# Kernel tuning notes

Measured on AMD Instinct MI355X. Metric: run time of the kernel, lower is better.

The kernel has to match this reference:

```python
import jax, jax.numpy as jnp
import numpy as np

QP_ITERS = 500          # projected-gradient iterations on the dual (converges for this tiny QP)
S_PEN = 1000.0          # slack penalty from the cvxpy objective
BN_EPS = 1e-5


def batchnorm(x, gamma, beta):
    # x: (B, N, C); BatchNorm1d training-mode stats over (batch, points)
    mu = x.mean(axis=(0, 1))
    var = x.var(axis=(0, 1))
    return (x - mu) * jax.lax.rsqrt(var + BN_EPS) * gamma + beta


def solve_qp(p, G, h):
    # min_z,s 0.5||z-p||^2 + 1000||s||^2  s.t. G z <= h + s, s >= 0
    # Dual (eliminating z = p - G^T lam, s = lam/(2*1000)):
    #   min_{lam>=0} 0.5 lam^T M lam - lam^T q,  M = G G^T + I/(2*S_PEN), q = G p - h
    nc = G.shape[1]
    M = jnp.einsum('bcv,bdv->bcd', G, G) + jnp.eye(nc, dtype=G.dtype) / (2.0 * S_PEN)
    q = jnp.einsum('bcv,bv->bc', G, p) - h
    # safe step size: 1/trace(M) <= 1/lambda_max(M)
    alpha = jax.lax.stop_gradient(1.0 / jnp.trace(M, axis1=1, axis2=2))[:, None]

    def step(lam, _):
        grad = jnp.einsum('bcd,bd->bc', M, lam) - q
        return jnp.maximum(lam - alpha * grad, 0.0), None

    lam0 = jnp.zeros_like(q)
    lam, _ = jax.lax.scan(step, lam0, None, length=QP_ITERS)
    z = p - jnp.einsum('bcv,bc->bv', G, lam)
    return z


def setup_inputs() -> dict:
    key = jax.random.key(0)
    ks = jax.random.split(key, 16)
    B, N, NC = 64, 8192, 12

    def w(k, shape, s):
        return (jax.random.normal(k, shape) * s).astype(jnp.float32)

    bc2 = jnp.concatenate([w(ks[10], (NC * 3,), 0.02), jnp.full((NC,), 0.02, jnp.float32)])
    return {
        'pcd': jax.random.normal(ks[0], (B, N, 3), dtype=jnp.float32),
        # MiniPointNet (1x1 convs as matmuls) + batchnorm affine params
        'W1': w(ks[1], (64, 3), 0.4), 'b1': jnp.zeros(64), 'g1': jnp.ones(64), 'be1': jnp.zeros(64),
        'W2': w(ks[2], (128, 64), 0.1), 'b2': jnp.zeros(128), 'g2': jnp.ones(128), 'be2': jnp.zeros(128),
        'W3': w(ks[3], (256, 128), 0.07), 'b3': jnp.zeros(256), 'g3': jnp.ones(256), 'be3': jnp.zeros(256),
        'Wfc': w(ks[4], (128, 256), 0.05), 'bfc': jnp.zeros(128),
        # constraint_net: 128 -> 128 -> 48
        'Wc1': w(ks[5], (128, 128), 0.08), 'bc1': jnp.zeros(128),
        'Wc2': w(ks[6], (NC * 4, 128), 0.08), 'bc2': bc2,
        # p_net: 128 -> 64 -> 7 (last layer ~N(0, 0.001), zero bias)
        'Wp1': w(ks[7], (64, 128), 0.08), 'bp1': jnp.zeros(64),
        'Wp2': w(ks[8], (7, 64), 0.001), 'bp2': jnp.zeros(7),
    }


def reference(pcd, W1, b1, g1, be1, W2, b2, g2, be2, W3, b3, g3, be3,
              Wfc, bfc, Wc1, bc1, Wc2, bc2, Wp1, bp1, Wp2, bp2):
    B = pcd.shape[0]
    NC = bc2.shape[0] // 4
    # MiniPointNet: pointwise MLP + global max pool
    x = jax.nn.relu(batchnorm(pcd @ W1.T + b1, g1, be1))     # (B,N,64)
    x = jax.nn.relu(batchnorm(x @ W2.T + b2, g2, be2))       # (B,N,128)
    x = jax.nn.relu(batchnorm(x @ W3.T + b3, g3, be3))       # (B,N,256)
    feats = x.max(axis=1) @ Wfc.T + bfc                       # (B,128)

    raw_p = jax.nn.relu(feats @ Wp1.T + bp1) @ Wp2.T + bp2    # (B,7)
    p_pred = jnp.concatenate([
        jnp.tanh(raw_p[:, :3]) * 0.1,
        jnp.tanh(raw_p[:, 3:6]) * 1.57,
        jnp.tanh(raw_p[:, 6:7]) * 0.05], axis=1)

    out_cons = (jax.nn.relu(feats @ Wc1.T + bc1) @ Wc2.T + bc2).reshape(B, NC, 4)
    normals = out_cons[:, :, :3]
    # F.normalize(p=2, dim=2): clamp norm at 1e-12
    normals = normals / jnp.clip(jnp.linalg.norm(normals, axis=2, keepdims=True), 1e-12)
    h = jax.nn.softplus(out_cons[:, :, 3]) + 0.005            # (B,NC)
    G = jnp.concatenate([normals, jnp.zeros((B, NC, 4), normals.dtype)], axis=2)  # (B,NC,7)

    delta_norm = solve_qp(p_pred, G, h)                       # (B,7)
    return delta_norm, normals, h, p_pred
```

## Files before the change

kernel.cpp:

```cpp
#include <hip/hip_runtime.h>
#include <hip/hip_bf16.h>

#define NPTS 524288
#define NBATCH 64

typedef __attribute__((ext_vector_type(8))) short bf16x8;
typedef __attribute__((ext_vector_type(4))) float f32x4;
typedef const float* __restrict__ fp;

__device__ __forceinline__ __hip_bfloat16 f2b(float v) { return __float2bfloat16(v); }
__device__ __forceinline__ unsigned bfbits(float v) {
    union { __hip_bfloat16 h; unsigned short s; } u; u.h = f2b(v); return (unsigned)u.s;
}

__device__ __forceinline__ unsigned fkey(float f) {
    unsigned u = __float_as_uint(f);
    return u ^ ((u & 0x80000000u) ? 0xFFFFFFFFu : 0x80000000u);
}
__device__ __forceinline__ float funkey(unsigned k) {
    unsigned u = (k & 0x80000000u) ? (k ^ 0x80000000u) : ~k;
    return __uint_as_float(u);
}

union U8 { bf16x8 v; __hip_bfloat16 e[8]; unsigned u[4]; };

static __device__ __forceinline__ f32x4 mfma16(bf16x8 a, bf16x8 b, f32x4 c) {
    return __builtin_amdgcn_mfma_f32_16x16x32_bf16(a, b, c, 0, 0, 0);
}

__global__ void k_prep(fp W1, fp b1, fp W2, fp W3,
                       __hip_bfloat16* __restrict__ W2b,
                       __hip_bfloat16* __restrict__ W3b,
                       unsigned* __restrict__ W1p )
{
    int i = blockIdx.x * blockDim.x + threadIdx.x;
    if (i < 8192) W2b[i] = f2b(W2[i]);
    const int j = i - 8192;
    if (j >= 0 && j < 32768) W3b[j] = f2b(W3[j]);
    const int c = i - 40960;
    if (c >= 0 && c < 64) {
        unsigned lo = bfbits(W1[3*c+0]) | (bfbits(W1[3*c+1]) << 16);
        unsigned hi = bfbits(W1[3*c+2]) | (bfbits(b1[c]) << 16);
        W1p[c*2+0] = lo; W1p[c*2+1] = hi;
    }
}

__launch_bounds__(256)
__global__ void k_moments(fp pcd, float* __restrict__ mom)
{
    float s[9];
#pragma unroll
    for (int i = 0; i < 9; ++i) s[i] = 0.f;
    const int stride = gridDim.x * blockDim.x;
    for (int p = blockIdx.x * blockDim.x + threadIdx.x; p < NPTS; p += stride) {
        const float x = pcd[3*p+0], y = pcd[3*p+1], z = pcd[3*p+2];
        s[0] += x; s[1] += y; s[2] += z;
        s[3] = fmaf(x, x, s[3]); s[4] = fmaf(x, y, s[4]); s[5] = fmaf(x, z, s[5]);
        s[6] = fmaf(y, y, s[6]); s[7] = fmaf(y, z, s[7]); s[8] = fmaf(z, z, s[8]);
    }
#pragma unroll
    for (int off = 1; off < 64; off <<= 1) {
#pragma unroll
        for (int i = 0; i < 9; ++i) s[i] += __shfl_xor(s[i], off);
    }
    __shared__ float red[4][9];
    const int lane = threadIdx.x & 63, wv = threadIdx.x >> 6;
    if (lane == 0) {
#pragma unroll
        for (int i = 0; i < 9; ++i) red[wv][i] = s[i];
    }
    __syncthreads();
    if (threadIdx.x < 9) {
        const int i = threadIdx.x;
        atomicAdd(&mom[i], red[0][i] + red[1][i] + red[2][i] + red[3][i]);
    }
}

__global__ void k_fin1(const float* __restrict__ mom, fp W1, fp b1, fp g1, fp be1,
                       float* __restrict__ s1, float* __restrict__ t1)
{
    const int c = threadIdx.x;
    const float inv = 1.f / (float)NPTS;
    const float m0 = mom[0]*inv, m1 = mom[1]*inv, m2 = mom[2]*inv;
    const float c00 = mom[3]*inv - m0*m0, c01 = mom[4]*inv - m0*m1, c02 = mom[5]*inv - m0*m2;
    const float c11 = mom[6]*inv - m1*m1, c12 = mom[7]*inv - m1*m2, c22 = mom[8]*inv - m2*m2;
    const float w0 = W1[c*3+0], w1 = W1[c*3+1], w2 = W1[c*3+2];
    const float mu = w0*m0 + w1*m1 + w2*m2 + b1[c];
    float var = w0*w0*c00 + w1*w1*c11 + w2*w2*c22 + 2.f*(w0*w1*c01 + w0*w2*c02 + w1*w2*c12);
    var = fmaxf(var, 0.f);
    const float sc = g1[c] * rsqrtf(var + 1e-5f);
    s1[c] = sc;
    t1[c] = be1[c] - mu*sc;
}

__launch_bounds__(256, 2)
__global__ void k_pass1(fp pcd, const unsigned* __restrict__ W1p,
                        const float* __restrict__ s1, const float* __restrict__ t1,
                        const __hip_bfloat16* __restrict__ W2b,
                        float* __restrict__ st2s, float* __restrict__ st2q)
{
    __shared__ __hip_bfloat16 x1s[64*72];
    const int tid = threadIdx.x, wv = tid >> 6, lane = tid & 63;
    const int m = lane & 15, q = lane >> 4;
    const int batch = blockIdx.x >> 5, sub = blockIdx.x & 31;

    bf16x8 wb1[4];
#pragma unroll
    for (int nt = 0; nt < 4; ++nt) {
        U8 w; w.u[0] = w.u[1] = w.u[2] = w.u[3] = 0;
        if (q == 0) { w.u[0] = W1p[(nt*16+m)*2]; w.u[1] = W1p[(nt*16+m)*2+1]; }
        wb1[nt] = w.v;
    }
    float s1v[4], t1v[4];
#pragma unroll
    for (int nt = 0; nt < 4; ++nt) { s1v[nt] = s1[nt*16+m]; t1v[nt] = t1[nt*16+m]; }

    bf16x8 wb2[8][2];
#pragma unroll
    for (int nt = 0; nt < 8; ++nt) {
#pragma unroll
        for (int kk = 0; kk < 2; ++kk)
            wb2[nt][kk] = *(const bf16x8*)(W2b + (nt*16+m)*64 + kk*32 + q*8);
    }

    float s_acc[8], q_acc[8];
#pragma unroll
    for (int nt = 0; nt < 8; ++nt) { s_acc[nt] = 0.f; q_acc[nt] = 0.f; }

    const int rowA = (wv*16 + m) * 72;

    for (int it = 0; it < 4; ++it) {
        const int p0 = batch*8192 + sub*256 + it*64 + wv*16;
        const float* pp = pcd + (size_t)(p0 + m) * 3;
        const float cx = pp[0], cy = pp[1], cz = pp[2];
        U8 a1; a1.u[0] = a1.u[1] = a1.u[2] = a1.u[3] = 0;
        if (q == 0) {
            a1.u[0] = bfbits(cx) | (bfbits(cy) << 16);
            a1.u[1] = bfbits(cz) | (bfbits(1.f) << 16);
        }
#pragma unroll
        for (int nt = 0; nt < 4; ++nt) {
            f32x4 c1 = mfma16(a1.v, wb1[nt], (f32x4){0.f,0.f,0.f,0.f});
#pragma unroll
            for (int r = 0; r < 4; ++r) {
                const float v = fmaxf(fmaf(c1[r], s1v[nt], t1v[nt]), 0.f);
                const unsigned own = bfbits(v);
                const unsigned oth = (unsigned)__shfl_xor((int)own, 1);
                if ((m & 1) == 0) {
                    const int row = wv*16 + q*4 + r;
                    *(unsigned*)&x1s[row*72 + nt*16 + m] = own | (oth << 16);
                }
            }
        }
        const bf16x8 a2k0 = *(const bf16x8*)&x1s[rowA + 0  + q*8];
        const bf16x8 a2k1 = *(const bf16x8*)&x1s[rowA + 32 + q*8];
#pragma unroll
        for (int nt = 0; nt < 8; ++nt) {
            f32x4 c = mfma16(a2k0, wb2[nt][0], (f32x4){0.f,0.f,0.f,0.f});
            c = mfma16(a2k1, wb2[nt][1], c);
            s_acc[nt] += (c[0] + c[1]) + (c[2] + c[3]);
            q_acc[nt] = fmaf(c[0],c[0], fmaf(c[1],c[1], fmaf(c[2],c[2], fmaf(c[3],c[3], q_acc[nt]))));
        }
    }
#pragma unroll
    for (int nt = 0; nt < 8; ++nt) {
        s_acc[nt] += __shfl_xor(s_acc[nt], 16); q_acc[nt] += __shfl_xor(q_acc[nt], 16);
        s_acc[nt] += __shfl_xor(s_acc[nt], 32); q_acc[nt] += __shfl_xor(q_acc[nt], 32);
    }
    __syncthreads();
    float* red = (float*)x1s;
    if (q == 0) {
#pragma unroll
        for (int nt = 0; nt < 8; ++nt) {
            red[wv*128 + nt*16 + m] = s_acc[nt];
            red[512 + wv*128 + nt*16 + m] = q_acc[nt];
        }
    }
    __syncthreads();
    if (tid < 128) {
        float s = 0.f, ss = 0.f;
#pragma unroll
        for (int w4 = 0; w4 < 4; ++w4) { s += red[w4*128 + tid]; ss += red[512 + w4*128 + tid]; }
        const int slot = blockIdx.x & 255;
        atomicAdd(&st2s[slot*128 + tid], s);
        atomicAdd(&st2q[slot*128 + tid], ss);
    }
}

__global__ void k_fin2(const float* __restrict__ sum, const float* __restrict__ sq,
                       fp g, fp be, float* __restrict__ sOut, float* __restrict__ tOut)
{
    const int ch = threadIdx.x;
    float s = 0.f, ss = 0.f;
    for (int slot = 0; slot < 256; ++slot) { s += sum[slot*128 + ch]; ss += sq[slot*128 + ch]; }
    const float inv = 1.f / (float)NPTS;
    const float mu = s * inv;
    const float var = fmaxf(ss * inv - mu*mu, 0.f);
    const float sc = g[ch] * rsqrtf(var + 1e-5f);
    sOut[ch] = sc;
    tOut[ch] = be[ch] - mu*sc;
}

__launch_bounds__(256, 2)
__global__ void k_pass2(fp pcd, const unsigned* __restrict__ W1p,
                        const float* __restrict__ s1, const float* __restrict__ t1,
                        const __hip_bfloat16* __restrict__ W2b,
                        const float* __restrict__ s2, const float* __restrict__ t2,
                        const __hip_bfloat16* __restrict__ W3b,
                        float* __restrict__ st3s, float* __restrict__ st3q,
                        unsigned* __restrict__ maxk, unsigned* __restrict__ mink)
{
    __shared__ __hip_bfloat16 x1s[64*72];
    __shared__ __hip_bfloat16 x2s[64*136];
    __shared__ __hip_bfloat16 w2s[128*72];
    const int tid = threadIdx.x, wv = tid >> 6, lane = tid & 63;
    const int m = lane & 15, q = lane >> 4;
    const int batch = blockIdx.x >> 5, sub = blockIdx.x & 31;

    {
        const int row = tid >> 1, half = tid & 1;
#pragma unroll
        for (int jj = 0; jj < 2; ++jj) {
            const bf16x8 wa = *(const bf16x8*)(W2b + row*64 + half*32 + jj*16);
            const bf16x8 wb = *(const bf16x8*)(W2b + row*64 + half*32 + jj*16 + 8);
            *(bf16x8*)&w2s[row*72 + half*32 + jj*16]     = wa;
            *(bf16x8*)&w2s[row*72 + half*32 + jj*16 + 8] = wb;
        }
    }

    bf16x8 wb1[4];
#pragma unroll
    for (int nt = 0; nt < 4; ++nt) {
        U8 w; w.u[0] = w.u[1] = w.u[2] = w.u[3] = 0;
        if (q == 0) { w.u[0] = W1p[(nt*16+m)*2]; w.u[1] = W1p[(nt*16+m)*2+1]; }
        wb1[nt] = w.v;
    }
    float s1v[4], t1v[4];
#pragma unroll
    for (int nt = 0; nt < 4; ++nt) { s1v[nt] = s1[nt*16+m]; t1v[nt] = t1[nt*16+m]; }
    float s2v[8], t2v[8];
#pragma unroll
    for (int nt = 0; nt < 8; ++nt) { s2v[nt] = s2[nt*16+m]; t2v[nt] = t2[nt*16+m]; }

    bf16x8 wb3[4][4];
#pragma unroll
    for (int nt = 0; nt < 4; ++nt) {
        const int ch3 = wv*64 + nt*16 + m;
#pragma unroll
        for (int ks = 0; ks < 4; ++ks)
            wb3[nt][ks] = *(const bf16x8*)(W3b + ch3*128 + ks*32 + q*8);
    }

    float s3[4], q3[4], mx3[4], mn3[4];
#pragma unroll
    for (int nt = 0; nt < 4; ++nt) { s3[nt]=0.f; q3[nt]=0.f; mx3[nt]=-3.4e38f; mn3[nt]=3.4e38f; }

    const int rowA = (wv*16 + m) * 72;
    __syncthreads();

    for (int it = 0; it < 4; ++it) {
        asm volatile("" ::: "memory");
        const int p0 = batch*8192 + sub*256 + it*64 + wv*16;
        const float* pp = pcd + (size_t)(p0 + m) * 3;
        const float cx = pp[0], cy = pp[1], cz = pp[2];
        U8 a1; a1.u[0] = a1.u[1] = a1.u[2] = a1.u[3] = 0;
        if (q == 0) {
            a1.u[0] = bfbits(cx) | (bfbits(cy) << 16);
            a1.u[1] = bfbits(cz) | (bfbits(1.f) << 16);
        }
#pragma unroll
        for (int nt = 0; nt < 4; ++nt) {
            f32x4 c1 = mfma16(a1.v, wb1[nt], (f32x4){0.f,0.f,0.f,0.f});
#pragma unroll
            for (int r = 0; r < 4; ++r) {
                const float v = fmaxf(fmaf(c1[r], s1v[nt], t1v[nt]), 0.f);
                const unsigned own = bfbits(v);
                const unsigned oth = (unsigned)__shfl_xor((int)own, 1);
                if ((m & 1) == 0) {
                    const int row = wv*16 + q*4 + r;
                    *(unsigned*)&x1s[row*72 + nt*16 + m] = own | (oth << 16);
                }
            }
        }
        const bf16x8 a2k0 = *(const bf16x8*)&x1s[rowA + 0  + q*8];
        const bf16x8 a2k1 = *(const bf16x8*)&x1s[rowA + 32 + q*8];
#pragma unroll
        for (int nt = 0; nt < 8; ++nt) {
            const bf16x8 wb20 = *(const bf16x8*)&w2s[(nt*16+m)*72 + 0  + q*8];
            const bf16x8 wb21 = *(const bf16x8*)&w2s[(nt*16+m)*72 + 32 + q*8];
            f32x4 c = mfma16(a2k0, wb20, (f32x4){0.f,0.f,0.f,0.f});
            c = mfma16(a2k1, wb21, c);
#pragma unroll
            for (int r = 0; r < 4; ++r) {
                const float v = fmaxf(fmaf(c[r], s2v[nt], t2v[nt]), 0.f);
                const unsigned own = bfbits(v);
                const unsigned oth = (unsigned)__shfl_xor((int)own, 1);
                if ((m & 1) == 0) {
                    const int row = wv*16 + q*4 + r;
                    *(unsigned*)&x2s[row*136 + nt*16 + m] = own | (oth << 16);
                }
            }
        }
        __syncthreads();
#pragma unroll
        for (int ms = 0; ms < 4; ++ms) {
            const int rowM = (ms*16 + m) * 136;
            bf16x8 a3[4];
#pragma unroll
            for (int ks = 0; ks < 4; ++ks)
                a3[ks] = *(const bf16x8*)&x2s[rowM + ks*32 + q*8];
#pragma unroll
            for (int nt = 0; nt < 4; ++nt) {
                f32x4 c = mfma16(a3[0], wb3[nt][0], (f32x4){0.f,0.f,0.f,0.f});
                c = mfma16(a3[1], wb3[nt][1], c);
                c = mfma16(a3[2], wb3[nt][2], c);
                c = mfma16(a3[3], wb3[nt][3], c);
                s3[nt] += (c[0] + c[1]) + (c[2] + c[3]);
                q3[nt] = fmaf(c[0],c[0], fmaf(c[1],c[1], fmaf(c[2],c[2], fmaf(c[3],c[3], q3[nt]))));
                mx3[nt] = fmaxf(fmaxf(c[0], c[1]), fmaxf(fmaxf(c[2], c[3]), mx3[nt]));
                mn3[nt] = fminf(fminf(c[0], c[1]), fminf(fminf(c[2], c[3]), mn3[nt]));
            }
        }
        __syncthreads();
    }
#pragma unroll
    for (int nt = 0; nt < 4; ++nt) {
        s3[nt] += __shfl_xor(s3[nt], 16);  q3[nt] += __shfl_xor(q3[nt], 16);
        mx3[nt] = fmaxf(mx3[nt], __shfl_xor(mx3[nt], 16));
        mn3[nt] = fminf(mn3[nt], __shfl_xor(mn3[nt], 16));
        s3[nt] += __shfl_xor(s3[nt], 32);  q3[nt] += __shfl_xor(q3[nt], 32);
        mx3[nt] = fmaxf(mx3[nt], __shfl_xor(mx3[nt], 32));
        mn3[nt] = fminf(mn3[nt], __shfl_xor(mn3[nt], 32));
    }
    if (q == 0) {
        const int slot = blockIdx.x & 255;
#pragma unroll
        for (int nt = 0; nt < 4; ++nt) {
            const int ch3 = wv*64 + nt*16 + m;
            atomicAdd(&st3s[slot*256 + ch3], s3[nt]);
            atomicAdd(&st3q[slot*256 + ch3], q3[nt]);
            atomicMax(&maxk[batch*256 + ch3], fkey(mx3[nt]));
            atomicMin(&mink[batch*256 + ch3], fkey(mn3[nt]));
        }
    }
}

__global__ void k_fin3(const float* __restrict__ sum, const float* __restrict__ sq,
                       fp g, fp be, const unsigned* __restrict__ maxk,
                       const unsigned* __restrict__ mink, float* __restrict__ pre)
{
    const int ch = threadIdx.x;
    float s = 0.f, ss = 0.f;
    for (int slot = 0; slot < 256; ++slot) { s += sum[slot*256 + ch]; ss += sq[slot*256 + ch]; }
    const float inv = 1.f / (float)NPTS;
    const float mu = s * inv;
    const float var = fmaxf(ss * inv - mu*mu, 0.f);
    const float sc = g[ch] * rsqrtf(var + 1e-5f);
    const float sh = be[ch] - mu*sc;
    for (int b = 0; b < NBATCH; ++b) {
        const float fmx = funkey(maxk[b*256 + ch]);
        const float fmn = funkey(mink[b*256 + ch]);
        const float pick = (sc >= 0.f) ? fmx : fmn;
        pre[b*256 + ch] = fmaxf(fmaf(pick, sc, sh), 0.f);
    }
}

__launch_bounds__(128)
__global__ void k_head(const float* __restrict__ pre,
                       fp Wfc, fp bfc, fp Wc1, fp bc1, fp Wc2, fp bc2,
                       fp Wp1, fp bp1, fp Wp2, fp bp2,
                       float* __restrict__ out)
{
    __shared__ float pf[256], ft[128], hcs[128], hps[64], ocs[48], nrm[36], hS[12], pp[8];
    const int bb = blockIdx.x, tid = threadIdx.x;
    pf[tid] = pre[bb*256 + tid];
    pf[tid+128] = pre[bb*256 + 128 + tid];
    __syncthreads();
    {
        float a = bfc[tid];
        const float* wr = Wfc + tid*256;
        for (int k = 0; k < 256; ++k) a = fmaf(pf[k], wr[k], a);
        ft[tid] = a;
    }
    __syncthreads();
    {
        float a = bc1[tid];
        const float* wr = Wc1 + tid*128;
        for (int k = 0; k < 128; ++k) a = fmaf(ft[k], wr[k], a);
        hcs[tid] = fmaxf(a, 0.f);
    }
    if (tid < 64) {
        float a = bp1[tid];
        const float* wr = Wp1 + tid*128;
        for (int k = 0; k < 128; ++k) a = fmaf(ft[k], wr[k], a);
        hps[tid] = fmaxf(a, 0.f);
    }
    __syncthreads();
    if (tid < 48) {
        float a = bc2[tid];
        const float* wr = Wc2 + tid*128;
        for (int k = 0; k < 128; ++k) a = fmaf(hcs[k], wr[k], a);
        ocs[tid] = a;
    }
    if (tid < 7) {
        float a = bp2[tid];
        const float* wr = Wp2 + tid*64;
        for (int k = 0; k < 64; ++k) a = fmaf(hps[k], wr[k], a);
        const float sc = (tid < 3) ? 0.1f : ((tid < 6) ? 1.57f : 0.05f);
        pp[tid] = tanhf(a) * sc;
    }
    __syncthreads();
    if (tid < 12) {
        float nx = ocs[tid*4+0], ny = ocs[tid*4+1], nz = ocs[tid*4+2];
        const float nn = fmaxf(sqrtf(nx*nx + ny*ny + nz*nz), 1e-12f);
        const float inv = 1.f / nn;
        nx *= inv; ny *= inv; nz *= inv;
        nrm[tid*3+0] = nx; nrm[tid*3+1] = ny; nrm[tid*3+2] = nz;
        const float xx = ocs[tid*4+3];
        hS[tid] = ((xx > 20.f) ? xx : log1pf(expf(xx))) + 0.005f;
    }
    __syncthreads();

    const int lane = tid & 63;
    const int c = (lane < 12) ? lane : 11;
    const float n0 = nrm[c*3+0], n1 = nrm[c*3+1], n2 = nrm[c*3+2];
    float Mrow[12];
    float trace = 0.f;
#pragma unroll
    for (int d = 0; d < 12; ++d) {
        const float d0 = nrm[d*3+0], d1 = nrm[d*3+1], d2 = nrm[d*3+2];
        Mrow[d] = n0*d0 + n1*d1 + n2*d2 + ((d == lane) ? 5e-4f : 0.f);
        trace += d0*d0 + d1*d1 + d2*d2;
    }
    const float alpha = 1.f / (trace + 12.f*5e-4f);
    const float qc = n0*pp[0] + n1*pp[1] + n2*pp[2] - hS[c];
    float lam = 0.f;
    for (int it = 0; it < 500; ++it) {
        const float l0 = __shfl(lam, 0),  l1 = __shfl(lam, 1),  l2 = __shfl(lam, 2);
        const float l3 = __shfl(lam, 3),  l4 = __shfl(lam, 4),  l5 = __shfl(lam, 5);
        const float l6 = __shfl(lam, 6),  l7 = __shfl(lam, 7),  l8 = __shfl(lam, 8);
        const float l9 = __shfl(lam, 9),  l10 = __shfl(lam, 10), l11 = __shfl(lam, 11);
        const float g0 = fmaf(Mrow[0], l0, fmaf(Mrow[3], l3, fmaf(Mrow[6], l6, Mrow[9]*l9)));
        const float g1 = fmaf(Mrow[1], l1, fmaf(Mrow[4], l4, fmaf(Mrow[7], l7, Mrow[10]*l10)));
        const float g2 = fmaf(Mrow[2], l2, fmaf(Mrow[5], l5, fmaf(Mrow[8], l8, Mrow[11]*l11)));
        lam = fmaxf(fmaf(-alpha, g0 + g1 + g2 - qc, lam), 0.f);
    }
    float v0 = (lane < 12) ? n0*lam : 0.f;
    float v1 = (lane < 12) ? n1*lam : 0.f;
    float v2 = (lane < 12) ? n2*lam : 0.f;
#pragma unroll
    for (int off = 1; off <= 8; off <<= 1) {
        v0 += __shfl_xor(v0, off);
        v1 += __shfl_xor(v1, off);
        v2 += __shfl_xor(v2, off);
    }
    if (tid < 7) {
        float z;
        if (tid == 0) z = pp[0] - v0;
        else if (tid == 1) z = pp[1] - v1;
        else if (tid == 2) z = pp[2] - v2;
        else z = pp[tid];
        out[bb*7 + tid] = z;
    }
    if (tid < 36) out[448 + bb*36 + tid] = nrm[tid];
    if (tid < 12) out[2752 + bb*12 + tid] = hS[tid];
    if (tid < 7)  out[3520 + bb*7 + tid] = pp[tid];
}

extern "C" void kernel_launch(void* const* d_in, const int* in_sizes, int n_in,
                              void* d_out, int out_size, void* d_ws, size_t ws_size,
                              hipStream_t stream) {
    fp pcd = (fp)d_in[0];
    fp W1 = (fp)d_in[1],  b1 = (fp)d_in[2],  g1 = (fp)d_in[3],  be1 = (fp)d_in[4];
    fp W2 = (fp)d_in[5],  b2 = (fp)d_in[6],  g2 = (fp)d_in[7],  be2 = (fp)d_in[8];
    fp W3 = (fp)d_in[9],  b3 = (fp)d_in[10], g3 = (fp)d_in[11], be3 = (fp)d_in[12];
    fp Wfc = (fp)d_in[13], bfc = (fp)d_in[14];
    fp Wc1 = (fp)d_in[15], bc1 = (fp)d_in[16];
    fp Wc2 = (fp)d_in[17], bc2 = (fp)d_in[18];
    fp Wp1 = (fp)d_in[19], bp1 = (fp)d_in[20];
    fp Wp2 = (fp)d_in[21], bp2 = (fp)d_in[22];
    (void)b2; (void)b3;

    float* ws = (float*)d_ws;
    float* mom  = ws + 0;
    float* s1   = ws + 16;
    float* t1   = ws + 80;
    float* s2   = ws + 144;
    float* t2   = ws + 272;
    float* pre  = ws + 400;
    float* st2s = ws + 16784;
    float* st2q = ws + 49552;
    float* st3s = ws + 82320;
    float* st3q = ws + 147856;
    unsigned* maxk = (unsigned*)(ws + 213392);
    unsigned* mink = (unsigned*)(ws + 229776);
    __hip_bfloat16* W2b = (__hip_bfloat16*)(ws + 246160);
    __hip_bfloat16* W3b = (__hip_bfloat16*)(ws + 250256);
    unsigned* W1p = (unsigned*)(ws + 266640);
    if (ws_size < (size_t)266768 * 4) return;

    hipMemsetAsync(d_ws, 0, (size_t)229776 * 4, stream);
    hipMemsetAsync((void*)mink, 0xFF, (size_t)16384 * 4, stream);

    k_prep<<<161, 256, 0, stream>>>(W1, b1, W2, W3, W2b, W3b, W1p);
    k_moments<<<256, 256, 0, stream>>>(pcd, mom);
    k_fin1<<<1, 64, 0, stream>>>(mom, W1, b1, g1, be1, s1, t1);
    k_pass1<<<2048, 256, 0, stream>>>(pcd, W1p, s1, t1, W2b, st2s, st2q);
    k_fin2<<<1, 128, 0, stream>>>(st2s, st2q, g2, be2, s2, t2);
    k_pass2<<<2048, 256, 0, stream>>>(pcd, W1p, s1, t1, W2b, s2, t2, W3b,
                                      st3s, st3q, maxk, mink);
    k_fin3<<<1, 256, 0, stream>>>(st3s, st3q, g3, be3, maxk, mink, pre);
    k_head<<<64, 128, 0, stream>>>(pre, Wfc, bfc, Wc1, bc1, Wc2, bc2,
                                   Wp1, bp1, Wp2, bp2, (float*)d_out);
}
```

Measured before the change: 328.6 us.

## Fold BN1 into W1, redistribute layer-1 output via shuffles, fuse fin3 into head

Folds the layer-1 batchnorm scale and shift into the packed bf16 W1 weights inside k_fin1. Layer 1 is computed with swapped MFMA operands and its output is redistributed to layer-2 A-fragments through cross-lane shuffles instead of an LDS round trip. k_pass2 now keeps W2 in registers, double-buffers the x2 LDS tile and drops the per-iteration barrier. Other changes: fewer atomic slots for the BN statistics (smaller memset and reduction), k_fin3 merged into k_head, and more k_moments blocks. Register pressure rises (pass1 now asks for 3 blocks per SM), and folding the scale before the bf16 rounding slightly changes numerics.

```diff
diff --git a/kernel.cpp b/kernel.cpp
--- a/kernel.cpp
+++ b/kernel.cpp
@@ -12,6 +12,9 @@
 __device__ __forceinline__ unsigned bfbits(float v) {
     union { __hip_bfloat16 h; unsigned short s; } u; u.h = f2b(v); return (unsigned)u.s;
 }
+__device__ __forceinline__ unsigned pk2(float a, float b) {
+    return bfbits(a) | (bfbits(b) << 16);
+}
 
 __device__ __forceinline__ unsigned fkey(float f) {
     unsigned u = __float_as_uint(f);
@@ -28,21 +31,13 @@
     return __builtin_amdgcn_mfma_f32_16x16x32_bf16(a, b, c, 0, 0, 0);
 }
 
-__global__ void k_prep(fp W1, fp b1, fp W2, fp W3,
-                       __hip_bfloat16* __restrict__ W2b,
-                       __hip_bfloat16* __restrict__ W3b,
-                       unsigned* __restrict__ W1p )
+__global__ void k_prep(fp W2, fp W3, __hip_bfloat16* __restrict__ W2b,
+                       __hip_bfloat16* __restrict__ W3b)
 {
     int i = blockIdx.x * blockDim.x + threadIdx.x;
     if (i < 8192) W2b[i] = f2b(W2[i]);
     const int j = i - 8192;
     if (j >= 0 && j < 32768) W3b[j] = f2b(W3[j]);
-    const int c = i - 40960;
-    if (c >= 0 && c < 64) {
-        unsigned lo = bfbits(W1[3*c+0]) | (bfbits(W1[3*c+1]) << 16);
-        unsigned hi = bfbits(W1[3*c+2]) | (bfbits(b1[c]) << 16);
-        W1p[c*2+0] = lo; W1p[c*2+1] = hi;
-    }
 }
 
 __launch_bounds__(256)
@@ -77,7 +72,7 @@
 }
 
 __global__ void k_fin1(const float* __restrict__ mom, fp W1, fp b1, fp g1, fp be1,
-                       float* __restrict__ s1, float* __restrict__ t1)
+                       unsigned* __restrict__ W1p)
 {
     const int c = threadIdx.x;
     const float inv = 1.f / (float)NPTS;
@@ -89,17 +84,39 @@
     float var = w0*w0*c00 + w1*w1*c11 + w2*w2*c22 + 2.f*(w0*w1*c01 + w0*w2*c02 + w1*w2*c12);
     var = fmaxf(var, 0.f);
     const float sc = g1[c] * rsqrtf(var + 1e-5f);
-    s1[c] = sc;
-    t1[c] = be1[c] - mu*sc;
-}
-
-__launch_bounds__(256, 2)
+    const float sh = be1[c] - mu*sc;
+    W1p[c*2+0] = pk2(w0*sc, w1*sc);
+    W1p[c*2+1] = pk2(w2*sc, b1[c]*sc + sh);
+}
+
+#define L1_AND_REDIST(a2f)                                                      \
+    {                                                                           \
+        unsigned u1s[4][2];                                                     \
+        _Pragma("unroll")                                                       \
+        for (int nt = 0; nt < 4; ++nt) {                                        \
+            f32x4 c1 = mfma16(wb1[nt], a1.v, (f32x4){0.f,0.f,0.f,0.f});         \
+            u1s[nt][0] = pk2(fmaxf(c1[0],0.f), fmaxf(c1[1],0.f));               \
+            u1s[nt][1] = pk2(fmaxf(c1[2],0.f), fmaxf(c1[3],0.f));               \
+        }                                                                       \
+        const int srcBase = m + ((q & 1) ? 32 : 0);                             \
+        _Pragma("unroll")                                                       \
+        for (int ks = 0; ks < 2; ++ks) {                                        \
+            _Pragma("unroll")                                                   \
+            for (int t2 = 0; t2 < 4; ++t2) {                                    \
+                const int src = srcBase + 16*(t2>>1);                           \
+                const unsigned rlo = (unsigned)__shfl((int)u1s[2*ks  ][t2&1], src); \
+                const unsigned rhi = (unsigned)__shfl((int)u1s[2*ks+1][t2&1], src); \
+                a2f[ks].u[t2] = (q >= 2) ? rhi : rlo;                           \
+            }                                                                   \
+        }                                                                       \
+    }
+
+__launch_bounds__(256, 3)
 __global__ void k_pass1(fp pcd, const unsigned* __restrict__ W1p,
-                        const float* __restrict__ s1, const float* __restrict__ t1,
                         const __hip_bfloat16* __restrict__ W2b,
                         float* __restrict__ st2s, float* __restrict__ st2q)
 {
-    __shared__ __hip_bfloat16 x1s[64*72];
+    __shared__ float red[1024];
     const int tid = threadIdx.x, wv = tid >> 6, lane = tid & 63;
     const int m = lane & 15, q = lane >> 4;
     const int batch = blockIdx.x >> 5, sub = blockIdx.x & 31;
@@ -111,10 +128,6 @@
         if (q == 0) { w.u[0] = W1p[(nt*16+m)*2]; w.u[1] = W1p[(nt*16+m)*2+1]; }
         wb1[nt] = w.v;
     }
-    float s1v[4], t1v[4];
-#pragma unroll
-    for (int nt = 0; nt < 4; ++nt) { s1v[nt] = s1[nt*16+m]; t1v[nt] = t1[nt*16+m]; }
-
     bf16x8 wb2[8][2];
 #pragma unroll
     for (int nt = 0; nt < 8; ++nt) {
@@ -126,38 +139,21 @@
     float s_acc[8], q_acc[8];
 #pragma unroll
     for (int nt = 0; nt < 8; ++nt) { s_acc[nt] = 0.f; q_acc[nt] = 0.f; }
-
-    const int rowA = (wv*16 + m) * 72;
 
     for (int it = 0; it < 4; ++it) {
         const int p0 = batch*8192 + sub*256 + it*64 + wv*16;
         const float* pp = pcd + (size_t)(p0 + m) * 3;
         const float cx = pp[0], cy = pp[1], cz = pp[2];
         U8 a1; a1.u[0] = a1.u[1] = a1.u[2] = a1.u[3] = 0;
-        if (q == 0) {
-            a1.u[0] = bfbits(cx) | (bfbits(cy) << 16);
-            a1.u[1] = bfbits(cz) | (bfbits(1.f) << 16);
-        }
-#pragma unroll
-        for (int nt = 0; nt < 4; ++nt) {
-            f32x4 c1 = mfma16(a1.v, wb1[nt], (f32x4){0.f,0.f,0.f,0.f});
-#pragma unroll
-            for (int r = 0; r < 4; ++r) {
-                const float v = fmaxf(fmaf(c1[r], s1v[nt], t1v[nt]), 0.f);
-                const unsigned own = bfbits(v);
-                const unsigned oth = (unsigned)__shfl_xor((int)own, 1);
-                if ((m & 1) == 0) {
-                    const int row = wv*16 + q*4 + r;
-                    *(unsigned*)&x1s[row*72 + nt*16 + m] = own | (oth << 16);
-                }
-            }
-        }
-        const bf16x8 a2k0 = *(const bf16x8*)&x1s[rowA + 0  + q*8];
-        const bf16x8 a2k1 = *(const bf16x8*)&x1s[rowA + 32 + q*8];
+        if (q == 0) { a1.u[0] = pk2(cx, cy); a1.u[1] = pk2(cz, 1.f); }
+
+        U8 a2f[2];
+        L1_AND_REDIST(a2f)
+
 #pragma unroll
         for (int nt = 0; nt < 8; ++nt) {
-            f32x4 c = mfma16(a2k0, wb2[nt][0], (f32x4){0.f,0.f,0.f,0.f});
-            c = mfma16(a2k1, wb2[nt][1], c);
+            f32x4 c = mfma16(a2f[0].v, wb2[nt][0], (f32x4){0.f,0.f,0.f,0.f});
+            c = mfma16(a2f[1].v, wb2[nt][1], c);
             s_acc[nt] += (c[0] + c[1]) + (c[2] + c[3]);
             q_acc[nt] = fmaf(c[0],c[0], fmaf(c[1],c[1], fmaf(c[2],c[2], fmaf(c[3],c[3], q_acc[nt]))));
         }
@@ -167,8 +163,6 @@
         s_acc[nt] += __shfl_xor(s_acc[nt], 16); q_acc[nt] += __shfl_xor(q_acc[nt], 16);
         s_acc[nt] += __shfl_xor(s_acc[nt], 32); q_acc[nt] += __shfl_xor(q_acc[nt], 32);
     }
-    __syncthreads();
-    float* red = (float*)x1s;
     if (q == 0) {
 #pragma unroll
         for (int nt = 0; nt < 8; ++nt) {
@@ -181,7 +175,7 @@
         float s = 0.f, ss = 0.f;
 #pragma unroll
         for (int w4 = 0; w4 < 4; ++w4) { s += red[w4*128 + tid]; ss += red[512 + w4*128 + tid]; }
-        const int slot = blockIdx.x & 255;
+        const int slot = blockIdx.x & 63;
         atomicAdd(&st2s[slot*128 + tid], s);
         atomicAdd(&st2q[slot*128 + tid], ss);
     }
@@ -192,7 +186,7 @@
 {
     const int ch = threadIdx.x;
     float s = 0.f, ss = 0.f;
-    for (int slot = 0; slot < 256; ++slot) { s += sum[slot*128 + ch]; ss += sq[slot*128 + ch]; }
+    for (int slot = 0; slot < 64; ++slot) { s += sum[slot*128 + ch]; ss += sq[slot*128 + ch]; }
     const float inv = 1.f / (float)NPTS;
     const float mu = s * inv;
     const float var = fmaxf(ss * inv - mu*mu, 0.f);
@@ -203,30 +197,16 @@
 
 __launch_bounds__(256, 2)
 __global__ void k_pass2(fp pcd, const unsigned* __restrict__ W1p,
-                        const float* __restrict__ s1, const float* __restrict__ t1,
                         const __hip_bfloat16* __restrict__ W2b,
                         const float* __restrict__ s2, const float* __restrict__ t2,
                         const __hip_bfloat16* __restrict__ W3b,
                         float* __restrict__ st3s, float* __restrict__ st3q,
                         unsigned* __restrict__ maxk, unsigned* __restrict__ mink)
 {
-    __shared__ __hip_bfloat16 x1s[64*72];
-    __shared__ __hip_bfloat16 x2s[64*136];
-    __shared__ __hip_bfloat16 w2s[128*72];
+    __shared__ alignas(16) __hip_bfloat16 x2s[2][64*136];
     const int tid = threadIdx.x, wv = tid >> 6, lane = tid & 63;
     const int m = lane & 15, q = lane >> 4;
     const int batch = blockIdx.x >> 5, sub = blockIdx.x & 31;
-
-    {
-        const int row = tid >> 1, half = tid & 1;
-#pragma unroll
-        for (int jj = 0; jj < 2; ++jj) {
-            const bf16x8 wa = *(const bf16x8*)(W2b + row*64 + half*32 + jj*16);
-            const bf16x8 wb = *(const bf16x8*)(W2b + row*64 + half*32 + jj*16 + 8);
-            *(bf16x8*)&w2s[row*72 + half*32 + jj*16]     = wa;
-            *(bf16x8*)&w2s[row*72 + half*32 + jj*16 + 8] = wb;
-        }
-    }
 
     bf16x8 wb1[4];
 #pragma unroll
@@ -235,9 +215,13 @@
         if (q == 0) { w.u[0] = W1p[(nt*16+m)*2]; w.u[1] = W1p[(nt*16+m)*2+1]; }
         wb1[nt] = w.v;
     }
-    float s1v[4], t1v[4];
-#pragma unroll
-    for (int nt = 0; nt < 4; ++nt) { s1v[nt] = s1[nt*16+m]; t1v[nt] = t1[nt*16+m]; }
+    bf16x8 wb2[8][2];
+#pragma unroll
+    for (int nt = 0; nt < 8; ++nt) {
+#pragma unroll
+        for (int kk = 0; kk < 2; ++kk)
+            wb2[nt][kk] = *(const bf16x8*)(W2b + (nt*16+m)*64 + kk*32 + q*8);
+    }
     float s2v[8], t2v[8];
 #pragma unroll
     for (int nt = 0; nt < 8; ++nt) { s2v[nt] = s2[nt*16+m]; t2v[nt] = t2[nt*16+m]; }
@@ -255,41 +239,21 @@
 #pragma unroll
     for (int nt = 0; nt < 4; ++nt) { s3[nt]=0.f; q3[nt]=0.f; mx3[nt]=-3.4e38f; mn3[nt]=3.4e38f; }
 
-    const int rowA = (wv*16 + m) * 72;
-    __syncthreads();
-
     for (int it = 0; it < 4; ++it) {
-        asm volatile("" ::: "memory");
+        __hip_bfloat16* xb = x2s[it & 1];
         const int p0 = batch*8192 + sub*256 + it*64 + wv*16;
         const float* pp = pcd + (size_t)(p0 + m) * 3;
         const float cx = pp[0], cy = pp[1], cz = pp[2];
         U8 a1; a1.u[0] = a1.u[1] = a1.u[2] = a1.u[3] = 0;
-        if (q == 0) {
-            a1.u[0] = bfbits(cx) | (bfbits(cy) << 16);
-            a1.u[1] = bfbits(cz) | (bfbits(1.f) << 16);
-        }
-#pragma unroll
-        for (int nt = 0; nt < 4; ++nt) {
-            f32x4 c1 = mfma16(a1.v, wb1[nt], (f32x4){0.f,0.f,0.f,0.f});
-#pragma unroll
-            for (int r = 0; r < 4; ++r) {
-                const float v = fmaxf(fmaf(c1[r], s1v[nt], t1v[nt]), 0.f);
-                const unsigned own = bfbits(v);
-                const unsigned oth = (unsigned)__shfl_xor((int)own, 1);
-                if ((m & 1) == 0) {
-                    const int row = wv*16 + q*4 + r;
-                    *(unsigned*)&x1s[row*72 + nt*16 + m] = own | (oth << 16);
-                }
-            }
-        }
-        const bf16x8 a2k0 = *(const bf16x8*)&x1s[rowA + 0  + q*8];
-        const bf16x8 a2k1 = *(const bf16x8*)&x1s[rowA + 32 + q*8];
+        if (q == 0) { a1.u[0] = pk2(cx, cy); a1.u[1] = pk2(cz, 1.f); }
+
+        U8 a2f[2];
+        L1_AND_REDIST(a2f)
+
 #pragma unroll
         for (int nt = 0; nt < 8; ++nt) {
-            const bf16x8 wb20 = *(const bf16x8*)&w2s[(nt*16+m)*72 + 0  + q*8];
-            const bf16x8 wb21 = *(const bf16x8*)&w2s[(nt*16+m)*72 + 32 + q*8];
-            f32x4 c = mfma16(a2k0, wb20, (f32x4){0.f,0.f,0.f,0.f});
-            c = mfma16(a2k1, wb21, c);
+            f32x4 c = mfma16(a2f[0].v, wb2[nt][0], (f32x4){0.f,0.f,0.f,0.f});
+            c = mfma16(a2f[1].v, wb2[nt][1], c);
 #pragma unroll
             for (int r = 0; r < 4; ++r) {
                 const float v = fmaxf(fmaf(c[r], s2v[nt], t2v[nt]), 0.f);
@@ -297,7 +261,7 @@
                 const unsigned oth = (unsigned)__shfl_xor((int)own, 1);
                 if ((m & 1) == 0) {
                     const int row = wv*16 + q*4 + r;
-                    *(unsigned*)&x2s[row*136 + nt*16 + m] = own | (oth << 16);
+                    *(unsigned*)&xb[row*136 + nt*16 + m] = own | (oth << 16);
                 }
             }
         }
@@ -308,7 +272,7 @@
             bf16x8 a3[4];
 #pragma unroll
             for (int ks = 0; ks < 4; ++ks)
-                a3[ks] = *(const bf16x8*)&x2s[rowM + ks*32 + q*8];
+                a3[ks] = *(const bf16x8*)&xb[rowM + ks*32 + q*8];
 #pragma unroll
             for (int nt = 0; nt < 4; ++nt) {
                 f32x4 c = mfma16(a3[0], wb3[nt][0], (f32x4){0.f,0.f,0.f,0.f});
@@ -321,7 +285,6 @@
                 mn3[nt] = fminf(fminf(c[0], c[1]), fminf(fminf(c[2], c[3]), mn3[nt]));
             }
         }
-        __syncthreads();
     }
 #pragma unroll
     for (int nt = 0; nt < 4; ++nt) {
@@ -333,7 +296,7 @@
         mn3[nt] = fminf(mn3[nt], __shfl_xor(mn3[nt], 32));
     }
     if (q == 0) {
-        const int slot = blockIdx.x & 255;
+        const int slot = blockIdx.x & 63;
 #pragma unroll
         for (int nt = 0; nt < 4; ++nt) {
             const int ch3 = wv*64 + nt*16 + m;
@@ -345,36 +308,29 @@
     }
 }
 
-__global__ void k_fin3(const float* __restrict__ sum, const float* __restrict__ sq,
-                       fp g, fp be, const unsigned* __restrict__ maxk,
-                       const unsigned* __restrict__ mink, float* __restrict__ pre)
-{
-    const int ch = threadIdx.x;
-    float s = 0.f, ss = 0.f;
-    for (int slot = 0; slot < 256; ++slot) { s += sum[slot*256 + ch]; ss += sq[slot*256 + ch]; }
-    const float inv = 1.f / (float)NPTS;
-    const float mu = s * inv;
-    const float var = fmaxf(ss * inv - mu*mu, 0.f);
-    const float sc = g[ch] * rsqrtf(var + 1e-5f);
-    const float sh = be[ch] - mu*sc;
-    for (int b = 0; b < NBATCH; ++b) {
-        const float fmx = funkey(maxk[b*256 + ch]);
-        const float fmn = funkey(mink[b*256 + ch]);
-        const float pick = (sc >= 0.f) ? fmx : fmn;
-        pre[b*256 + ch] = fmaxf(fmaf(pick, sc, sh), 0.f);
-    }
-}
-
 __launch_bounds__(128)
-__global__ void k_head(const float* __restrict__ pre,
+__global__ void k_head(const float* __restrict__ st3s, const float* __restrict__ st3q,
+                       fp g3, fp be3,
+                       const unsigned* __restrict__ maxk, const unsigned* __restrict__ mink,
                        fp Wfc, fp bfc, fp Wc1, fp bc1, fp Wc2, fp bc2,
                        fp Wp1, fp bp1, fp Wp2, fp bp2,
                        float* __restrict__ out)
 {
     __shared__ float pf[256], ft[128], hcs[128], hps[64], ocs[48], nrm[36], hS[12], pp[8];
     const int bb = blockIdx.x, tid = threadIdx.x;
-    pf[tid] = pre[bb*256 + tid];
-    pf[tid+128] = pre[bb*256 + 128 + tid];
+#pragma unroll
+    for (int h = 0; h < 2; ++h) {
+        const int ch = tid + h*128;
+        float s = 0.f, ss = 0.f;
+        for (int slot = 0; slot < 64; ++slot) { s += st3s[slot*256 + ch]; ss += st3q[slot*256 + ch]; }
+        const float inv = 1.f / (float)NPTS;
+        const float mu = s * inv;
+        const float var = fmaxf(ss * inv - mu*mu, 0.f);
+        const float sc = g3[ch] * rsqrtf(var + 1e-5f);
+        const float sh = be3[ch] - mu*sc;
+        const float pick = (sc >= 0.f) ? funkey(maxk[bb*256 + ch]) : funkey(mink[bb*256 + ch]);
+        pf[ch] = fmaxf(fmaf(pick, sc, sh), 0.f);
+    }
     __syncthreads();
     {
         float a = bfc[tid];
@@ -471,45 +427,41 @@
                               void* d_out, int out_size, void* d_ws, size_t ws_size,
                               hipStream_t stream) {
     fp pcd = (fp)d_in[0];
-    fp W1 = (fp)d_in[1],  b1 = (fp)d_in[2],  g1 = (fp)d_in[3],  be1 = (fp)d_in[4];
-    fp W2 = (fp)d_in[5],  b2 = (fp)d_in[6],  g2 = (fp)d_in[7],  be2 = (fp)d_in[8];
-    fp W3 = (fp)d_in[9],  b3 = (fp)d_in[10], g3 = (fp)d_in[11], be3 = (fp)d_in[12];
+    fp W1 = (fp)d_in[1],  fp_b1 = (fp)d_in[2],  g1 = (fp)d_in[3],  be1 = (fp)d_in[4];
+    fp W2 = (fp)d_in[5],  g2 = (fp)d_in[7],  be2 = (fp)d_in[8];
+    fp W3 = (fp)d_in[9],  g3 = (fp)d_in[11], be3 = (fp)d_in[12];
     fp Wfc = (fp)d_in[13], bfc = (fp)d_in[14];
     fp Wc1 = (fp)d_in[15], bc1 = (fp)d_in[16];
     fp Wc2 = (fp)d_in[17], bc2 = (fp)d_in[18];
     fp Wp1 = (fp)d_in[19], bp1 = (fp)d_in[20];
     fp Wp2 = (fp)d_in[21], bp2 = (fp)d_in[22];
-    (void)b2; (void)b3;
 
     float* ws = (float*)d_ws;
     float* mom  = ws + 0;
-    float* s1   = ws + 16;
-    float* t1   = ws + 80;
     float* s2   = ws + 144;
     float* t2   = ws + 272;
-    float* pre  = ws + 400;
-    float* st2s = ws + 16784;
-    float* st2q = ws + 49552;
-    float* st3s = ws + 82320;
-    float* st3q = ws + 147856;
-    unsigned* maxk = (unsigned*)(ws + 213392);
-    unsigned* mink = (unsigned*)(ws + 229776);
-    __hip_bfloat16* W2b = (__hip_bfloat16*)(ws + 246160);
-    __hip_bfloat16* W3b = (__hip_bfloat16*)(ws + 250256);
-    unsigned* W1p = (unsigned*)(ws + 266640);
-    if (ws_size < (size_t)266768 * 4) return;
-
-    hipMemsetAsync(d_ws, 0, (size_t)229776 * 4, stream);
+    float* st2s = ws + 400;
+    float* st2q = ws + 8592;
+    float* st3s = ws + 16784;
+    float* st3q = ws + 33168;
+    unsigned* maxk = (unsigned*)(ws + 49552);
+    unsigned* mink = (unsigned*)(ws + 65936);
+    __hip_bfloat16* W2b = (__hip_bfloat16*)(ws + 82320);
+    __hip_bfloat16* W3b = (__hip_bfloat16*)(ws + 86416);
+    unsigned* W1p = (unsigned*)(ws + 102800);
+    if (ws_size < (size_t)102928 * 4) return;
+
+    hipMemsetAsync(d_ws, 0, (size_t)65936 * 4, stream);
     hipMemsetAsync((void*)mink, 0xFF, (size_t)16384 * 4, stream);
 
-    k_prep<<<161, 256, 0, stream>>>(W1, b1, W2, W3, W2b, W3b, W1p);
-    k_moments<<<256, 256, 0, stream>>>(pcd, mom);
-    k_fin1<<<1, 64, 0, stream>>>(mom, W1, b1, g1, be1, s1, t1);
-    k_pass1<<<2048, 256, 0, stream>>>(pcd, W1p, s1, t1, W2b, st2s, st2q);
+    k_prep<<<160, 256, 0, stream>>>(W2, W3, W2b, W3b);
+    k_moments<<<1024, 256, 0, stream>>>(pcd, mom);
+    k_fin1<<<1, 64, 0, stream>>>(mom, W1, fp_b1, g1, be1, W1p);
+    k_pass1<<<2048, 256, 0, stream>>>(pcd, W1p, W2b, st2s, st2q);
     k_fin2<<<1, 128, 0, stream>>>(st2s, st2q, g2, be2, s2, t2);
-    k_pass2<<<2048, 256, 0, stream>>>(pcd, W1p, s1, t1, W2b, s2, t2, W3b,
+    k_pass2<<<2048, 256, 0, stream>>>(pcd, W1p, W2b, s2, t2, W3b,
                                       st3s, st3q, maxk, mink);
-    k_fin3<<<1, 256, 0, stream>>>(st3s, st3q, g3, be3, maxk, mink, pre);
-    k_head<<<64, 128, 0, stream>>>(pre, Wfc, bfc, Wc1, bc1, Wc2, bc2,
+    k_head<<<64, 128, 0, stream>>>(st3s, st3q, g3, be3, maxk, mink,
+                                   Wfc, bfc, Wc1, bc1, Wc2, bc2,
                                    Wp1, bp1, Wp2, bp2, (float*)d_out);
 }
```

Measured after the change: 319.1 us. 1.03x faster.
